# Optimization experiments

Measured on AMD Instinct MI355X. Metric: run time of the kernel, lower is better.

## Reference

```python
import jax, jax.numpy as jnp
import numpy as np

NUM_DEM = 2
VOCAB = 10000
EMB = 128


def setup_inputs() -> dict:
    key = jax.random.key(0)
    k_src, k_emb, k_w1, k_w2 = jax.random.split(key, 4)
    B = 16384
    # 0/1 multi-hot style input (demographic cols also 0/1; math identical)
    src = jax.random.randint(k_src, (B, NUM_DEM + VOCAB), 0, 2).astype(jnp.float32)
    embed = jax.random.normal(k_emb, (VOCAB, EMB), dtype=jnp.float32)
    W1 = jax.random.normal(k_w1, (NUM_DEM + EMB, 16), dtype=jnp.float32) * 0.1
    b1 = jnp.full((16,), 0.01, dtype=jnp.float32)
    W2 = jax.random.normal(k_w2, (16, 2), dtype=jnp.float32) * 0.1
    b2 = jnp.full((2,), 0.01, dtype=jnp.float32)
    return {"src": src, "embed": embed, "W1": W1, "b1": b1, "W2": W2, "b2": b2}


def reference(src, embed, W1, b1, W2, b2):
    dem = src[:, :NUM_DEM]                         # [B, 2]
    codes = src[:, NUM_DEM:].astype(jnp.int32)     # [B, V]
    mask = (codes != 0).astype(embed.dtype)        # multi-hot indicator [B, V]
    counts = jnp.sum(mask, axis=1, keepdims=True)  # [B, 1]
    # fused multi-hot gather + mean pooling (embedding-bag mean)
    pooled = (mask @ embed) / counts               # [B, EMB]
    x = jnp.concatenate([dem, pooled], axis=1)     # [B, 2+EMB]
    h = jnp.tanh(x @ W1 + b1)
    return h @ W2 + b2                             # [B, 2]
```

## Files before the change

### kernel.cpp

```cpp
#include <hip/hip_runtime.h>

#define NUM_DEM 2
#define VOCAB 10000
#define EMB 128
#define NROWS 16384
#define ROWLEN (NUM_DEM + VOCAB)
#define KSTEPS 313
#define PCOLS 132
#define BPACK_USHORTS ((size_t)KSTEPS * 4096)
#define BPACK_BYTES (BPACK_USHORTS * 2)
#define NCH 4

typedef float f32x4 __attribute__((ext_vector_type(4)));
typedef __bf16 bf16x8 __attribute__((ext_vector_type(8)));
typedef short s16x8 __attribute__((ext_vector_type(8)));

union Frag {
    s16x8 s;
    bf16x8 b;
    unsigned int u[4];
};

__device__ __forceinline__ unsigned short f2bf_rtne(float f) {
    unsigned int u = __float_as_uint(f);
    u += 0x7FFFu + ((u >> 16) & 1u);
    return (unsigned short)(u >> 16);
}

__global__ void pack_embed_k(const float* __restrict__ embed,
                             unsigned short* __restrict__ bp) {
    int id = blockIdx.x * blockDim.x + threadIdx.x;
    if (id >= KSTEPS * 8 * 64) return;
    int l = id & 63;
    int c = (id >> 6) & 7;
    int t = id >> 9;
    int kbase = t * 32 + ((l >> 4) * 8);
    int n = c * 16 + (l & 15);
    unsigned short v[8];
#pragma unroll
    for (int j = 0; j < 8; ++j) {
        int k = kbase + j;
        float f = (k < VOCAB) ? embed[(size_t)k * EMB + n] : 0.0f;
        v[j] = f2bf_rtne(f);
    }
    uint4 w;
    w.x = (unsigned int)v[0] | ((unsigned int)v[1] << 16);
    w.y = (unsigned int)v[2] | ((unsigned int)v[3] << 16);
    w.z = (unsigned int)v[4] | ((unsigned int)v[5] << 16);
    w.w = (unsigned int)v[6] | ((unsigned int)v[7] << 16);
    *reinterpret_cast<uint4*>(bp + (size_t)id * 8) = w;
}

typedef const __attribute__((address_space(1))) unsigned int* gas_u32p;
typedef __attribute__((address_space(3))) unsigned int* las_u32p;
#define GLOAD_LDS16(g, l)                                                              \
    __builtin_amdgcn_global_load_lds((gas_u32p)(g), (las_u32p)(l), 16, 0, 0)

#define PERM_A(dst, x0, x1)                                                            \
    dst.u[0] = __builtin_amdgcn_perm(__float_as_uint(x0.y), __float_as_uint(x0.x),     \
                                     0x07060302u);                                     \
    dst.u[1] = __builtin_amdgcn_perm(__float_as_uint(x0.w), __float_as_uint(x0.z),     \
                                     0x07060302u);                                     \
    dst.u[2] = __builtin_amdgcn_perm(__float_as_uint(x1.y), __float_as_uint(x1.x),     \
                                     0x07060302u);                                     \
    dst.u[3] = __builtin_amdgcn_perm(__float_as_uint(x1.w), __float_as_uint(x1.z),     \
                                     0x07060302u);

__global__ __launch_bounds__(512, 4) void main_gemm_k(
    const float* __restrict__ src, const unsigned short* __restrict__ bp,
    float* __restrict__ part, int nch) {
    __shared__ alignas(16) unsigned short ldsB[2 * 4096];

    const int tid = threadIdx.x;
    const int lane = tid & 63;
    const int wid = tid >> 6;
    const int rb = blockIdx.x & 127;
    const int ch = blockIdx.x >> 7;
    const int t0 = (KSTEPS * ch) / nch;
    const int t1 = (KSTEPS * (ch + 1)) / nch;

    const int rowbase = rb * 128 + wid * 16;
    const int arow = rowbase + (lane & 15);
    const int kgrp8 = (lane >> 4) * 8;
    const float* asrc = src + (size_t)arow * ROWLEN + NUM_DEM + kgrp8;

    f32x4 pacc[8];
#pragma unroll
    for (int f = 0; f < 8; ++f) pacc[f] = (f32x4){0.f, 0.f, 0.f, 0.f};
    f32x4 cacc = (f32x4){0.f, 0.f, 0.f, 0.f};

    Frag onesf;
    {
        unsigned short o = ((lane & 15) == 0) ? (unsigned short)0x3F80 : (unsigned short)0;
        unsigned int ow = (unsigned int)o | ((unsigned int)o << 16);
        onesf.u[0] = ow; onesf.u[1] = ow; onesf.u[2] = ow; onesf.u[3] = ow;
    }

    int t = t0;
    for (; t + 2 <= t1; t += 2) {
        {
            const unsigned short* gB = bp + (size_t)t * 4096 + tid * 8;
            unsigned short* lB = ldsB + tid * 8;
            GLOAD_LDS16(gB, lB);
            GLOAD_LDS16(gB + 4096, lB + 4096);
        }

        Frag af0, af1;
        {
            f32x4 z = (f32x4){0.f, 0.f, 0.f, 0.f};
            f32x4 a00 = z, a01 = z, a10 = z, a11 = z;
            if (t * 32 + kgrp8 + 8 <= VOCAB) {
                const f32x4* ap = reinterpret_cast<const f32x4*>(asrc + (size_t)t * 32);
                a00 = ap[0];
                a01 = ap[1];
            }
            if ((t + 1) * 32 + kgrp8 + 8 <= VOCAB) {
                const f32x4* ap =
                    reinterpret_cast<const f32x4*>(asrc + (size_t)(t + 1) * 32);
                a10 = ap[0];
                a11 = ap[1];
            }
            PERM_A(af0, a00, a01);
            PERM_A(af1, a10, a11);
        }

        __syncthreads();

#pragma unroll
        for (int f = 0; f < 8; ++f) {
            Frag bfr;
            bfr.s = *reinterpret_cast<const s16x8*>(ldsB + f * 512 + lane * 8);
            pacc[f] = __builtin_amdgcn_mfma_f32_16x16x32_bf16(af0.b, bfr.b, pacc[f], 0, 0, 0);
        }
        cacc = __builtin_amdgcn_mfma_f32_16x16x32_bf16(af0.b, onesf.b, cacc, 0, 0, 0);
#pragma unroll
        for (int f = 0; f < 8; ++f) {
            Frag bfr;
            bfr.s = *reinterpret_cast<const s16x8*>(ldsB + 4096 + f * 512 + lane * 8);
            pacc[f] = __builtin_amdgcn_mfma_f32_16x16x32_bf16(af1.b, bfr.b, pacc[f], 0, 0, 0);
        }
        cacc = __builtin_amdgcn_mfma_f32_16x16x32_bf16(af1.b, onesf.b, cacc, 0, 0, 0);

        __syncthreads();
    }
    if (t < t1) {
        {
            const unsigned short* gB = bp + (size_t)t * 4096 + tid * 8;
            GLOAD_LDS16(gB, ldsB + tid * 8);
        }
        Frag af0;
        {
            f32x4 z = (f32x4){0.f, 0.f, 0.f, 0.f};
            f32x4 a00 = z, a01 = z;
            if (t * 32 + kgrp8 + 8 <= VOCAB) {
                const f32x4* ap = reinterpret_cast<const f32x4*>(asrc + (size_t)t * 32);
                a00 = ap[0];
                a01 = ap[1];
            }
            PERM_A(af0, a00, a01);
        }
        __syncthreads();
#pragma unroll
        for (int f = 0; f < 8; ++f) {
            Frag bfr;
            bfr.s = *reinterpret_cast<const s16x8*>(ldsB + f * 512 + lane * 8);
            pacc[f] = __builtin_amdgcn_mfma_f32_16x16x32_bf16(af0.b, bfr.b, pacc[f], 0, 0, 0);
        }
        cacc = __builtin_amdgcn_mfma_f32_16x16x32_bf16(af0.b, onesf.b, cacc, 0, 0, 0);
        __syncthreads();
    }

    const int rlo = (lane >> 4) * 4;
    float* pch = part + (size_t)ch * NROWS * PCOLS;
#pragma unroll
    for (int f = 0; f < 8; ++f) {
#pragma unroll
        for (int r = 0; r < 4; ++r) {
            int row = rowbase + rlo + r;
            pch[(size_t)row * PCOLS + f * 16 + (lane & 15)] = pacc[f][r];
        }
    }
    if ((lane & 15) == 0) {
#pragma unroll
        for (int r = 0; r < 4; ++r) {
            int row = rowbase + rlo + r;
            pch[(size_t)row * PCOLS + 128] = cacc[r];
        }
    }
}

__global__ __launch_bounds__(256) void mlp_k(const float* __restrict__ part,
                                             const float* __restrict__ src,
                                             const float* __restrict__ W1,
                                             const float* __restrict__ b1,
                                             const float* __restrict__ W2,
                                             const float* __restrict__ b2,
                                             float* __restrict__ out, int nch) {
    __shared__ float xls[16][131];
    __shared__ float hls[16][16];
    __shared__ float cnt[16];
    const int tid = threadIdx.x;
    const int rb = blockIdx.x * 16;

    if (tid < 16) {
        float s = 0.f;
        for (int c = 0; c < nch; ++c)
            s += part[((size_t)c * NROWS + rb + tid) * PCOLS + 128];
        cnt[tid] = s;
    }
    if (tid >= 16 && tid < 48) {
        int r = (tid - 16) >> 1, d = (tid - 16) & 1;
        xls[r][d] = src[(size_t)(rb + r) * ROWLEN + d];
    }
    __syncthreads();

    for (int idx = tid; idx < 16 * 128; idx += 256) {
        int r = idx >> 7, col = idx & 127;
        float s = 0.f;
        for (int c = 0; c < nch; ++c)
            s += part[((size_t)c * NROWS + rb + r) * PCOLS + col];
        xls[r][NUM_DEM + col] = s / cnt[r];
    }
    __syncthreads();

    {
        int r = tid >> 4, u = tid & 15;
        float acc = b1[u];
        for (int i = 0; i < NUM_DEM + EMB; ++i) acc += xls[r][i] * W1[i * 16 + u];
        hls[r][u] = tanhf(acc);
    }
    __syncthreads();

    if (tid < 32) {
        int r = tid >> 1, o = tid & 1;
        float acc = b2[o];
#pragma unroll
        for (int u = 0; u < 16; ++u) acc += hls[r][u] * W2[u * 2 + o];
        out[(size_t)(rb + r) * 2 + o] = acc;
    }
}

extern "C" void kernel_launch(void* const* d_in, const int* in_sizes, int n_in,
                              void* d_out, int out_size, void* d_ws, size_t ws_size,
                              hipStream_t stream) {
    const float* src = (const float*)d_in[0];
    const float* embed = (const float*)d_in[1];
    const float* W1 = (const float*)d_in[2];
    const float* b1 = (const float*)d_in[3];
    const float* W2 = (const float*)d_in[4];
    const float* b2 = (const float*)d_in[5];
    float* out = (float*)d_out;

    unsigned short* bpack = (unsigned short*)d_ws;
    float* part = (float*)((char*)d_ws + BPACK_BYTES);

    const size_t part1 = (size_t)NROWS * PCOLS * sizeof(float);
    int nch = NCH;
    while (nch > 1 && BPACK_BYTES + part1 * (size_t)nch > ws_size) nch >>= 1;

    hipLaunchKernelGGL(pack_embed_k, dim3((KSTEPS * 8 * 64 + 255) / 256), dim3(256), 0,
                       stream, embed, bpack);
    hipLaunchKernelGGL(main_gemm_k, dim3(128 * nch), dim3(512), 0, stream, src, bpack,
                       part, nch);
    hipLaunchKernelGGL(mlp_k, dim3(NROWS / 16), dim3(256), 0, stream, part, src, W1, b1,
                       W2, b2, out, nch);
}
```

Before: 197.2 us.

## Process two 128-row tiles per block to reuse LDS B tiles, double K-splits

Each block now computes 256 rows (two 16-row fragments per wave) against every staged embedding tile, so each B tile loaded into LDS serves twice as many MFMAs. To keep the grid size the same, the K dimension is split into 8 chunks instead of 4, and the partial-output row stride is narrowed from 132 to 129 columns. In exchange, register pressure roughly doubles for the accumulators, and there is more partial-sum traffic for the MLP kernel to reduce. Because the A matrix is fp32 src read straight from HBM, the load is likely bound by A bandwidth, so the extra B reuse may matter less than it appears.

```diff
diff --git a/kernel.cpp b/kernel.cpp
--- a/kernel.cpp
+++ b/kernel.cpp
@@ -6,10 +6,10 @@
 #define NROWS 16384
 #define ROWLEN (NUM_DEM + VOCAB)
 #define KSTEPS 313
-#define PCOLS 132
+#define PCOLS 129
 #define BPACK_USHORTS ((size_t)KSTEPS * 4096)
 #define BPACK_BYTES (BPACK_USHORTS * 2)
-#define NCH 4
+#define NCH 8
 
 typedef float f32x4 __attribute__((ext_vector_type(4)));
 typedef __bf16 bf16x8 __attribute__((ext_vector_type(8)));
@@ -66,6 +66,25 @@
     dst.u[3] = __builtin_amdgcn_perm(__float_as_uint(x1.w), __float_as_uint(x1.z),     \
                                      0x07060302u);
 
+#define LOAD_A_PAIR(AP, T, D0, D1)                                                     \
+    {                                                                                  \
+        f32x4 z = (f32x4){0.f, 0.f, 0.f, 0.f};                                         \
+        f32x4 a00 = z, a01 = z, a10 = z, a11 = z;                                      \
+        if ((T)*32 + kgrp8 + 8 <= VOCAB) {                                             \
+            const f32x4* ap = reinterpret_cast<const f32x4*>((AP) + (size_t)(T)*32);   \
+            a00 = ap[0];                                                               \
+            a01 = ap[1];                                                               \
+        }                                                                              \
+        if (((T) + 1) * 32 + kgrp8 + 8 <= VOCAB) {                                     \
+            const f32x4* ap =                                                          \
+                reinterpret_cast<const f32x4*>((AP) + (size_t)((T) + 1) * 32);         \
+            a10 = ap[0];                                                               \
+            a11 = ap[1];                                                               \
+        }                                                                              \
+        PERM_A(D0, a00, a01);                                                          \
+        PERM_A(D1, a10, a11);                                                          \
+    }
+
 __global__ __launch_bounds__(512, 4) void main_gemm_k(
     const float* __restrict__ src, const unsigned short* __restrict__ bp,
     float* __restrict__ part, int nch) {
@@ -74,20 +93,25 @@
     const int tid = threadIdx.x;
     const int lane = tid & 63;
     const int wid = tid >> 6;
-    const int rb = blockIdx.x & 127;
-    const int ch = blockIdx.x >> 7;
+    const int rb = blockIdx.x & 63;
+    const int ch = blockIdx.x >> 6;
     const int t0 = (KSTEPS * ch) / nch;
     const int t1 = (KSTEPS * (ch + 1)) / nch;
 
-    const int rowbase = rb * 128 + wid * 16;
-    const int arow = rowbase + (lane & 15);
+    const int rowbase0 = rb * 256 + wid * 16;
+    const int rowbase1 = rowbase0 + 128;
     const int kgrp8 = (lane >> 4) * 8;
-    const float* asrc = src + (size_t)arow * ROWLEN + NUM_DEM + kgrp8;
-
-    f32x4 pacc[8];
-#pragma unroll
-    for (int f = 0; f < 8; ++f) pacc[f] = (f32x4){0.f, 0.f, 0.f, 0.f};
-    f32x4 cacc = (f32x4){0.f, 0.f, 0.f, 0.f};
+    const float* asrc0 = src + (size_t)(rowbase0 + (lane & 15)) * ROWLEN + NUM_DEM + kgrp8;
+    const float* asrc1 = src + (size_t)(rowbase1 + (lane & 15)) * ROWLEN + NUM_DEM + kgrp8;
+
+    f32x4 pacc0[8], pacc1[8];
+#pragma unroll
+    for (int f = 0; f < 8; ++f) {
+        pacc0[f] = (f32x4){0.f, 0.f, 0.f, 0.f};
+        pacc1[f] = (f32x4){0.f, 0.f, 0.f, 0.f};
+    }
+    f32x4 cacc0 = (f32x4){0.f, 0.f, 0.f, 0.f};
+    f32x4 cacc1 = cacc0;
 
     Frag onesf;
     {
@@ -105,68 +129,63 @@
             GLOAD_LDS16(gB + 4096, lB + 4096);
         }
 
-        Frag af0, af1;
+        Frag af00, af01, af10, af11;
+        LOAD_A_PAIR(asrc0, t, af00, af01);
+        LOAD_A_PAIR(asrc1, t, af10, af11);
+
+        __syncthreads();
+
+#pragma unroll
+        for (int f = 0; f < 8; ++f) {
+            Frag bfr;
+            bfr.s = *reinterpret_cast<const s16x8*>(ldsB + f * 512 + lane * 8);
+            pacc0[f] = __builtin_amdgcn_mfma_f32_16x16x32_bf16(af00.b, bfr.b, pacc0[f], 0, 0, 0);
+            pacc1[f] = __builtin_amdgcn_mfma_f32_16x16x32_bf16(af10.b, bfr.b, pacc1[f], 0, 0, 0);
+        }
+        cacc0 = __builtin_amdgcn_mfma_f32_16x16x32_bf16(af00.b, onesf.b, cacc0, 0, 0, 0);
+        cacc1 = __builtin_amdgcn_mfma_f32_16x16x32_bf16(af10.b, onesf.b, cacc1, 0, 0, 0);
+#pragma unroll
+        for (int f = 0; f < 8; ++f) {
+            Frag bfr;
+            bfr.s = *reinterpret_cast<const s16x8*>(ldsB + 4096 + f * 512 + lane * 8);
+            pacc0[f] = __builtin_amdgcn_mfma_f32_16x16x32_bf16(af01.b, bfr.b, pacc0[f], 0, 0, 0);
+            pacc1[f] = __builtin_amdgcn_mfma_f32_16x16x32_bf16(af11.b, bfr.b, pacc1[f], 0, 0, 0);
+        }
+        cacc0 = __builtin_amdgcn_mfma_f32_16x16x32_bf16(af01.b, onesf.b, cacc0, 0, 0, 0);
+        cacc1 = __builtin_amdgcn_mfma_f32_16x16x32_bf16(af11.b, onesf.b, cacc1, 0, 0, 0);
+
+        __syncthreads();
+    }
+    if (t < t1) {
+        {
+            const unsigned short* gB = bp + (size_t)t * 4096 + tid * 8;
+            GLOAD_LDS16(gB, ldsB + tid * 8);
+        }
+        Frag af0t, af1t;
         {
             f32x4 z = (f32x4){0.f, 0.f, 0.f, 0.f};
             f32x4 a00 = z, a01 = z, a10 = z, a11 = z;
             if (t * 32 + kgrp8 + 8 <= VOCAB) {
-                const f32x4* ap = reinterpret_cast<const f32x4*>(asrc + (size_t)t * 32);
+                const f32x4* ap = reinterpret_cast<const f32x4*>(asrc0 + (size_t)t * 32);
                 a00 = ap[0];
                 a01 = ap[1];
+                const f32x4* aq = reinterpret_cast<const f32x4*>(asrc1 + (size_t)t * 32);
+                a10 = aq[0];
+                a11 = aq[1];
             }
-            if ((t + 1) * 32 + kgrp8 + 8 <= VOCAB) {
-                const f32x4* ap =
-                    reinterpret_cast<const f32x4*>(asrc + (size_t)(t + 1) * 32);
-                a10 = ap[0];
-                a11 = ap[1];
-            }
-            PERM_A(af0, a00, a01);
-            PERM_A(af1, a10, a11);
-        }
-
-        __syncthreads();
-
+            PERM_A(af0t, a00, a01);
+            PERM_A(af1t, a10, a11);
+        }
+        __syncthreads();
 #pragma unroll
         for (int f = 0; f < 8; ++f) {
             Frag bfr;
             bfr.s = *reinterpret_cast<const s16x8*>(ldsB + f * 512 + lane * 8);
-            pacc[f] = __builtin_amdgcn_mfma_f32_16x16x32_bf16(af0.b, bfr.b, pacc[f], 0, 0, 0);
-        }
-        cacc = __builtin_amdgcn_mfma_f32_16x16x32_bf16(af0.b, onesf.b, cacc, 0, 0, 0);
-#pragma unroll
-        for (int f = 0; f < 8; ++f) {
-            Frag bfr;
-            bfr.s = *reinterpret_cast<const s16x8*>(ldsB + 4096 + f * 512 + lane * 8);
-            pacc[f] = __builtin_amdgcn_mfma_f32_16x16x32_bf16(af1.b, bfr.b, pacc[f], 0, 0, 0);
-        }
-        cacc = __builtin_amdgcn_mfma_f32_16x16x32_bf16(af1.b, onesf.b, cacc, 0, 0, 0);
-
-        __syncthreads();
-    }
-    if (t < t1) {
-        {
-            const unsigned short* gB = bp + (size_t)t * 4096 + tid * 8;
-            GLOAD_LDS16(gB, ldsB + tid * 8);
-        }
-        Frag af0;
-        {
-            f32x4 z = (f32x4){0.f, 0.f, 0.f, 0.f};
-            f32x4 a00 = z, a01 = z;
-            if (t * 32 + kgrp8 + 8 <= VOCAB) {
-                const f32x4* ap = reinterpret_cast<const f32x4*>(asrc + (size_t)t * 32);
-                a00 = ap[0];
-                a01 = ap[1];
-            }
-            PERM_A(af0, a00, a01);
-        }
-        __syncthreads();
-#pragma unroll
-        for (int f = 0; f < 8; ++f) {
-            Frag bfr;
-            bfr.s = *reinterpret_cast<const s16x8*>(ldsB + f * 512 + lane * 8);
-            pacc[f] = __builtin_amdgcn_mfma_f32_16x16x32_bf16(af0.b, bfr.b, pacc[f], 0, 0, 0);
-        }
-        cacc = __builtin_amdgcn_mfma_f32_16x16x32_bf16(af0.b, onesf.b, cacc, 0, 0, 0);
+            pacc0[f] = __builtin_amdgcn_mfma_f32_16x16x32_bf16(af0t.b, bfr.b, pacc0[f], 0, 0, 0);
+            pacc1[f] = __builtin_amdgcn_mfma_f32_16x16x32_bf16(af1t.b, bfr.b, pacc1[f], 0, 0, 0);
+        }
+        cacc0 = __builtin_amdgcn_mfma_f32_16x16x32_bf16(af0t.b, onesf.b, cacc0, 0, 0, 0);
+        cacc1 = __builtin_amdgcn_mfma_f32_16x16x32_bf16(af1t.b, onesf.b, cacc1, 0, 0, 0);
         __syncthreads();
     }
 
@@ -176,15 +195,15 @@
     for (int f = 0; f < 8; ++f) {
 #pragma unroll
         for (int r = 0; r < 4; ++r) {
-            int row = rowbase + rlo + r;
-            pch[(size_t)row * PCOLS + f * 16 + (lane & 15)] = pacc[f][r];
+            pch[(size_t)(rowbase0 + rlo + r) * PCOLS + f * 16 + (lane & 15)] = pacc0[f][r];
+            pch[(size_t)(rowbase1 + rlo + r) * PCOLS + f * 16 + (lane & 15)] = pacc1[f][r];
         }
     }
     if ((lane & 15) == 0) {
 #pragma unroll
         for (int r = 0; r < 4; ++r) {
-            int row = rowbase + rlo + r;
-            pch[(size_t)row * PCOLS + 128] = cacc[r];
+            pch[(size_t)(rowbase0 + rlo + r) * PCOLS + 128] = cacc0[r];
+            pch[(size_t)(rowbase1 + rlo + r) * PCOLS + 128] = cacc1[r];
         }
     }
 }
@@ -260,7 +279,7 @@
 
     hipLaunchKernelGGL(pack_embed_k, dim3((KSTEPS * 8 * 64 + 255) / 256), dim3(256), 0,
                        stream, embed, bpack);
-    hipLaunchKernelGGL(main_gemm_k, dim3(128 * nch), dim3(512), 0, stream, src, bpack,
+    hipLaunchKernelGGL(main_gemm_k, dim3(64 * nch), dim3(512), 0, stream, src, bpack,
                        part, nch);
     hipLaunchKernelGGL(mlp_k, dim3(NROWS / 16), dim3(256), 0, stream, part, src, W1, b1,
                        W2, b2, out, nch);
```

New measurement: 208.6 us. 5.8% more time.
